# Optimization experiments

Hardware: AMD Instinct MI355X
Metric: run time of the kernel (lower is better)

Reference implementation:

```python
import jax, jax.numpy as jnp
import numpy as np

N = 100000       # nodes
E = 1200000      # edges
D_IN = 64
D_OUT = 64
ALPHA = 0.01     # LeakyReLU negative slope
EPS = 1e-5       # BatchNorm eps


def setup_inputs() -> dict:
    key = jax.random.key(0)
    k0, k1, k2, k3 = jax.random.split(key, 4)
    x = jax.random.normal(k0, (N, D_IN), dtype=jnp.float32)
    edge_idx = jax.random.randint(k1, (2, E), 0, N)
    edge_attr = jax.random.uniform(k2, (E,), dtype=jnp.float32)
    W = jax.random.normal(k3, (D_IN, D_OUT), dtype=jnp.float32) * (1.0 / np.sqrt(D_IN))
    b = jnp.zeros((D_OUT,), dtype=jnp.float32)
    gamma = jnp.ones((D_OUT,), dtype=jnp.float32)
    beta = jnp.zeros((D_OUT,), dtype=jnp.float32)
    return {"x": x, "edge_idx": edge_idx, "edge_attr": edge_attr,
            "W": W, "b": b, "gamma": gamma, "beta": beta}


def reference(x, edge_idx, edge_attr, W, b, gamma, beta):
    n = x.shape[0]
    row, col = edge_idx[0], edge_idx[1]
    # --- GCNConv: add self-loops, symmetric normalization ---
    loops = jnp.arange(n)
    row_f = jnp.concatenate([row, loops])                       # [E+N]
    col_f = jnp.concatenate([col, loops])                       # [E+N]
    w_f = jnp.concatenate([edge_attr, jnp.ones((n,), x.dtype)])  # [E+N]
    deg = jax.ops.segment_sum(w_f, col_f, num_segments=n)       # [N]
    deg_safe = jnp.where(deg > 0, deg, 1.0)
    dis = jnp.where(deg > 0, jax.lax.rsqrt(deg_safe), 0.0)      # deg^-1/2
    norm = dis[row_f] * w_f * dis[col_f]                        # [E+N]
    h = x @ W                                                   # [N, D_OUT]
    msg = norm[:, None] * h[row_f]                              # gather + scale
    agg = jax.ops.segment_sum(msg, col_f, num_segments=n) + b   # scatter-add
    # --- BatchNorm (training-mode batch stats, biased var) ---
    mean = jnp.mean(agg, axis=0)
    var = jnp.mean((agg - mean) ** 2, axis=0)
    hn = (agg - mean) * jax.lax.rsqrt(var + EPS) * gamma + beta
    # --- LeakyReLU ---
    return jnp.where(hn >= 0, hn, ALPHA * hn)
```

## Files before the change

### kernel.cpp

```cpp
#include <hip/hip_runtime.h>

#define D 64
#define ALPHA 0.01f
#define EPS 1e-5f
#define NREP 8
#define CAP 48
#define GSZ 128
#define GMAX 1024
#define NB 256

typedef __attribute__((ext_vector_type(8))) short short8;
typedef __attribute__((ext_vector_type(4))) float f32x4;

__device__ inline unsigned short f2bf(float f) {
    unsigned u = __float_as_uint(f);
    u += 0x7fffu + ((u >> 16) & 1u);
    return (unsigned short)(u >> 16);
}
__device__ inline float bf2f(unsigned short h) { return __uint_as_float((unsigned)h << 16); }

__global__ __launch_bounds__(256) void k_prepA(const float4* __restrict__ x4,
                                               ushort4* __restrict__ xb4,
                                               float* __restrict__ stats,
                                               const int* __restrict__ col,
                                               int* __restrict__ cnt_gb,
                                               long long n16, int G, int E) {
    __shared__ int h[GMAX];
    if (blockIdx.x < NB) {
        int b = blockIdx.x;
        for (int i = threadIdx.x; i < G; i += 256) h[i] = 0;
        __syncthreads();
        int chunk = (E + NB - 1) / NB;
        int e0 = b * chunk;
        int e1 = e0 + chunk; if (e1 > E) e1 = E;
        for (int e = e0 + threadIdx.x; e < e1; e += 256)
            atomicAdd(&h[col[e] >> 7], 1);
        __syncthreads();
        for (int i = threadIdx.x; i < G; i += 256)
            cnt_gb[i * NB + b] = h[i];
    } else {
        long long i = (long long)(blockIdx.x - NB) * 256 + threadIdx.x;
        if (i < n16) {
            float4 v = x4[i];
            ushort4 r;
            r.x = f2bf(v.x); r.y = f2bf(v.y); r.z = f2bf(v.z); r.w = f2bf(v.w);
            xb4[i] = r;
        }
        if (i < NREP * 128) stats[i] = 0.0f;
    }
}

__global__ __launch_bounds__(256) void k_scanA(const int* __restrict__ cnt_gb,
                                               int* __restrict__ bsum, int M) {
    __shared__ int ls[256];
    int base = blockIdx.x * 1024 + threadIdx.x * 4;
    int s = 0;
    if (base + 3 < M) {
        int4 v = *(const int4*)&cnt_gb[base];
        s = v.x + v.y + v.z + v.w;
    } else {
#pragma unroll
        for (int k = 0; k < 4; ++k) { int idx = base + k; if (idx < M) s += cnt_gb[idx]; }
    }
    ls[threadIdx.x] = s;
    __syncthreads();
    for (int off = 128; off > 0; off >>= 1) {
        if (threadIdx.x < off) ls[threadIdx.x] += ls[threadIdx.x + off];
        __syncthreads();
    }
    if (threadIdx.x == 0) bsum[blockIdx.x] = ls[0];
}

__global__ __launch_bounds__(256) void k_scanC(const int* __restrict__ cnt_gb,
                                               const int* __restrict__ bsum,
                                               int* __restrict__ pos,
                                               int* __restrict__ gseg, int M, int G, int E) {
    __shared__ int ls[256];
    int t = threadIdx.x;
    ls[t] = (t < blockIdx.x) ? bsum[t] : 0;
    __syncthreads();
    for (int off = 128; off > 0; off >>= 1) {
        if (t < off) ls[t] += ls[t + off];
        __syncthreads();
    }
    int base_total = ls[0];
    __syncthreads();
    int base = blockIdx.x * 1024 + t * 4;
    int v[4];
    int s = 0;
#pragma unroll
    for (int k = 0; k < 4; ++k) { int idx = base + k; v[k] = (idx < M) ? cnt_gb[idx] : 0; s += v[k]; }
    ls[t] = s;
    __syncthreads();
    int own = s;
    for (int off = 1; off < 256; off <<= 1) {
        int tv = (t >= off) ? ls[t - off] : 0;
        __syncthreads();
        ls[t] += tv;
        __syncthreads();
    }
    int excl = ls[t] - own + base_total;
#pragma unroll
    for (int k = 0; k < 4; ++k) {
        int idx = base + k;
        if (idx < M) {
            pos[idx] = excl;
            if ((idx & (NB - 1)) == 0) gseg[idx >> 8] = excl;
        }
        excl += v[k];
    }
    if (blockIdx.x == 0 && t == 0) gseg[G] = E;
}

__global__ __launch_bounds__(256) void k_binB(const int* __restrict__ eidx,
                                              const float* __restrict__ w,
                                              const int* __restrict__ pos,
                                              uint2* __restrict__ seg, int G, int E) {
    __shared__ int cursor[GMAX];
    int b = blockIdx.x;
    for (int g = threadIdx.x; g < G; g += 256) cursor[g] = pos[g * NB + b];
    __syncthreads();
    int chunk = (E + NB - 1) / NB;
    int e0 = b * chunk;
    int e1 = e0 + chunk; if (e1 > E) e1 = E;
    for (int e = e0 + threadIdx.x; e < e1; e += 256) {
        int row = eidx[e];
        int c = eidx[E + e];
        unsigned wq = (unsigned)(w[e] * 32767.0f + 0.5f);
        int slot = atomicAdd(&cursor[c >> 7], 1);
        seg[slot] = make_uint2((wq << 17) | (unsigned)row, (unsigned)(c & (GSZ - 1)));
    }
}

__global__ __launch_bounds__(256) void k_binC(const uint2* __restrict__ seg,
                                              const int* __restrict__ gseg,
                                              unsigned* __restrict__ bucket,
                                              int* __restrict__ cnt,
                                              float* __restrict__ dis,
                                              float* __restrict__ dis_s, int n) {
    __shared__ int cl[GSZ];
    __shared__ float ws[GSZ];
    int g = blockIdx.x;
    if (threadIdx.x < GSZ) { cl[threadIdx.x] = 0; ws[threadIdx.x] = 0.0f; }
    __syncthreads();
    int s0 = gseg[g], s1 = gseg[g + 1];
    for (int i = s0 + threadIdx.x; i < s1; i += 256) {
        uint2 ev = seg[i];
        int cig = (int)ev.y;
        int rank = atomicAdd(&cl[cig], 1);
        atomicAdd(&ws[cig], (float)(ev.x >> 17) * (1.0f / 32767.0f));
        int node = g * GSZ + cig;
        if (rank < CAP) bucket[(size_t)node * CAP + rank] = ev.x;
    }
    __syncthreads();
    if (threadIdx.x < GSZ) {
        int node = g * GSZ + threadIdx.x;
        if (node < n) {
            cnt[node] = cl[threadIdx.x];
            float d = rsqrtf(1.0f + ws[threadIdx.x]);
            dis[node] = d;
            dis_s[node] = d * (1.0f / 32767.0f);
        }
    }
}

__global__ __launch_bounds__(256) void k_gather(const unsigned short* __restrict__ xb,
                                                const unsigned* __restrict__ bucket,
                                                const int* __restrict__ cnt,
                                                const float* __restrict__ dis,
                                                const float* __restrict__ dis_s,
                                                unsigned short* __restrict__ aggb, int n) {
    int node = blockIdx.x * 4 + (threadIdx.x >> 6);
    if (node >= n) return;
    int lane = threadIdx.x & 63;
    int g = lane >> 3;
    int l = lane & 7;
    int c = cnt[node];
    if (c > CAP) c = CAP;
    float di = dis[node];
    float acc[8] = {0, 0, 0, 0, 0, 0, 0, 0};
    if (g == 0) {
        short8 xv = *(const short8*)(xb + ((size_t)node << 6) + l * 8);
#pragma unroll
        for (int k = 0; k < 8; ++k) acc[k] = bf2f((unsigned short)xv[k]) * di;
    }
    const unsigned* bkt = bucket + (size_t)node * CAP;
    int j0 = g, j1 = g + 8;
    unsigned v0 = (j0 < c) ? bkt[j0] : 0u;
    unsigned v1 = (j1 < c) ? bkt[j1] : 0u;
    while (j0 < c) {
        int p0 = j0 + 16, p1 = j1 + 16;
        unsigned w0 = (p0 < c) ? bkt[p0] : 0u;
        unsigned w1 = (p1 < c) ? bkt[p1] : 0u;
        int s0 = (int)(v0 & 0x1FFFFu);
        int s1 = (int)(v1 & 0x1FFFFu);
        float nr0 = (float)(v0 >> 17) * dis_s[s0];
        float nr1 = (float)(v1 >> 17) * dis_s[s1];
        short8 x0 = *(const short8*)(xb + ((size_t)s0 << 6) + l * 8);
        short8 x1 = *(const short8*)(xb + ((size_t)s1 << 6) + l * 8);
#pragma unroll
        for (int k = 0; k < 8; ++k) acc[k] += nr0 * bf2f((unsigned short)x0[k]);
#pragma unroll
        for (int k = 0; k < 8; ++k) acc[k] += nr1 * bf2f((unsigned short)x1[k]);
        v0 = w0; v1 = w1; j0 = p0; j1 = p1;
    }
#pragma unroll
    for (int off = 8; off <= 32; off <<= 1)
#pragma unroll
        for (int k = 0; k < 8; ++k) acc[k] += __shfl_xor(acc[k], off, 64);
    if (g == 0) {
        short8 r;
#pragma unroll
        for (int k = 0; k < 8; ++k) r[k] = (short)f2bf(acc[k] * di);
        *(short8*)(aggb + ((size_t)node << 6) + l * 8) = r;
    }
}

__global__ __launch_bounds__(256) void k_gemmstats(const unsigned short* __restrict__ aggb,
                                                   const float* __restrict__ Wm,
                                                   float* __restrict__ out,
                                                   float* __restrict__ stats, int n) {
    __shared__ unsigned short Wt[64 * 64];
    __shared__ float ssum[4][64], qsum[4][64];
    int tid = threadIdx.x;
    for (int i = tid; i < 4096; i += 256) {
        int k = i >> 6, nn = i & 63;
        Wt[nn * 64 + k] = f2bf(Wm[i]);
    }
    __syncthreads();
    int wv = tid >> 6;
    int lane = tid & 63;
    int l15 = lane & 15;
    int quad = lane >> 4;

    short8 bfrag[2][4];
#pragma unroll
    for (int h = 0; h < 2; ++h)
#pragma unroll
        for (int g = 0; g < 4; ++g)
            bfrag[h][g] = *(const short8*)&Wt[(g * 16 + l15) * 64 + h * 32 + quad * 8];

    float s[4] = {0, 0, 0, 0}, q[4] = {0, 0, 0, 0};
    int nwt = (n + 15) >> 4;
    for (int wt = blockIdx.x * 4 + wv; wt < nwt; wt += gridDim.x * 4) {
        int row0 = wt * 16;
        int arow = row0 + l15;
        if (arow >= n) arow = n - 1;
        const unsigned short* ap = aggb + (size_t)arow * 64 + quad * 8;
        short8 a0 = *(const short8*)ap;
        short8 a1 = *(const short8*)(ap + 32);
        f32x4 acc[4] = {{0, 0, 0, 0}, {0, 0, 0, 0}, {0, 0, 0, 0}, {0, 0, 0, 0}};
#pragma unroll
        for (int g = 0; g < 4; ++g) {
            acc[g] = __builtin_amdgcn_mfma_f32_16x16x32_bf16(a0, bfrag[0][g], acc[g], 0, 0, 0);
            acc[g] = __builtin_amdgcn_mfma_f32_16x16x32_bf16(a1, bfrag[1][g], acc[g], 0, 0, 0);
        }
#pragma unroll
        for (int r = 0; r < 4; ++r) {
            int row = row0 + quad * 4 + r;
            if (row < n) {
                size_t base = (size_t)row * 64;
#pragma unroll
                for (int g = 0; g < 4; ++g) {
                    float v = acc[g][r];
                    out[base + g * 16 + l15] = v;
                    s[g] += v;
                    q[g] += v * v;
                }
            }
        }
    }
#pragma unroll
    for (int off = 16; off <= 32; off <<= 1) {
#pragma unroll
        for (int g = 0; g < 4; ++g) {
            s[g] += __shfl_xor(s[g], off, 64);
            q[g] += __shfl_xor(q[g], off, 64);
        }
    }
    if (quad == 0) {
#pragma unroll
        for (int g = 0; g < 4; ++g) { ssum[wv][g * 16 + l15] = s[g]; qsum[wv][g * 16 + l15] = q[g]; }
    }
    __syncthreads();
    float* st = stats + (blockIdx.x & (NREP - 1)) * 128;
    if (tid < 64)
        atomicAdd(&st[tid], ssum[0][tid] + ssum[1][tid] + ssum[2][tid] + ssum[3][tid]);
    else if (tid < 128) {
        int t = tid - 64;
        atomicAdd(&st[64 + t], qsum[0][t] + qsum[1][t] + qsum[2][t] + qsum[3][t]);
    }
}

__global__ __launch_bounds__(256) void k_norm(float4* __restrict__ out4,
                                              const float* __restrict__ stats,
                                              const float* __restrict__ gamma,
                                              const float* __restrict__ beta, int n) {
    __shared__ float scale[64], shift[64];
    if (threadIdx.x < 64) {
        float sm = 0.0f, qm = 0.0f;
#pragma unroll
        for (int r = 0; r < NREP; ++r) {
            sm += stats[r * 128 + threadIdx.x];
            qm += stats[r * 128 + 64 + threadIdx.x];
        }
        float inv_n = 1.0f / (float)n;
        float mean = sm * inv_n;
        float var = qm * inv_n - mean * mean;
        float sc = rsqrtf(var + EPS) * gamma[threadIdx.x];
        scale[threadIdx.x] = sc;
        shift[threadIdx.x] = beta[threadIdx.x] - mean * sc;
    }
    __syncthreads();
    long long idx = (long long)blockIdx.x * blockDim.x + threadIdx.x;
    if (idx < (long long)n * 16) {
        int l = (int)(idx & 15);
        float4 v = out4[idx];
        float4 r;
        float a, b2;
        a = scale[l * 4 + 0]; b2 = shift[l * 4 + 0]; r.x = v.x * a + b2; r.x = r.x >= 0.0f ? r.x : ALPHA * r.x;
        a = scale[l * 4 + 1]; b2 = shift[l * 4 + 1]; r.y = v.y * a + b2; r.y = r.y >= 0.0f ? r.y : ALPHA * r.y;
        a = scale[l * 4 + 2]; b2 = shift[l * 4 + 2]; r.z = v.z * a + b2; r.z = r.z >= 0.0f ? r.z : ALPHA * r.z;
        a = scale[l * 4 + 3]; b2 = shift[l * 4 + 3]; r.w = v.w * a + b2; r.w = r.w >= 0.0f ? r.w : ALPHA * r.w;
        out4[idx] = r;
    }
}

extern "C" void kernel_launch(void* const* d_in, const int* in_sizes, int n_in,
                              void* d_out, int out_size, void* d_ws, size_t ws_size,
                              hipStream_t stream) {
    const float* x     = (const float*)d_in[0];
    const int*   eidx  = (const int*)d_in[1];
    const float* eattr = (const float*)d_in[2];
    const float* Wm    = (const float*)d_in[3];
    const float* gamma = (const float*)d_in[5];
    const float* beta  = (const float*)d_in[6];
    float* out = (float*)d_out;

    int n = in_sizes[0] / D;
    int E = in_sizes[2];
    int G = (n + GSZ - 1) / GSZ;
    int M = G * NB;
    int nbs = (M + 1023) / 1024;

    char* p = (char*)d_ws;
    uint2* seg = (uint2*)p;                     p += (size_t)E * 8;
    unsigned* bucket = (unsigned*)p;            p += (size_t)n * CAP * 4;
    unsigned short* xb   = (unsigned short*)p;  p += (size_t)n * D * 2;
    unsigned short* aggb = (unsigned short*)p;  p += (size_t)n * D * 2;
    int* cnt = (int*)p;                         p += (size_t)n * 4;
    float* dis = (float*)p;                     p += (size_t)n * 4;
    float* dis_s = (float*)p;                   p += (size_t)n * 4;
    float* stats = (float*)p;                   p += NREP * 128 * 4;
    int* cnt_gb = (int*)p;                      p += (size_t)M * 4;
    int* pos = (int*)p;                         p += (size_t)M * 4;
    int* gseg = (int*)p;                        p += ((size_t)G + 1) * 4;
    int* bsum = (int*)p;                        p += 256 * 4;

    long long n16 = (long long)n * 16;
    unsigned prep_blocks = (unsigned)((n16 + 255) / 256);

    k_prepA<<<NB + prep_blocks, 256, 0, stream>>>(
        (const float4*)x, (ushort4*)xb, stats, eidx + E, cnt_gb, n16, G, E);
    k_scanA<<<nbs, 256, 0, stream>>>(cnt_gb, bsum, M);
    k_scanC<<<nbs, 256, 0, stream>>>(cnt_gb, bsum, pos, gseg, M, G, E);
    k_binB<<<NB, 256, 0, stream>>>(eidx, eattr, pos, seg, G, E);
    k_binC<<<G, 256, 0, stream>>>(seg, gseg, bucket, cnt, dis, dis_s, n);
    k_gather<<<(n + 3) / 4, 256, 0, stream>>>(xb, bucket, cnt, dis, dis_s, aggb, n);
    k_gemmstats<<<1024, 256, 0, stream>>>(aggb, Wm, out, stats, n);
    k_norm<<<(unsigned)((n16 + 255) / 256), 256, 0, stream>>>(
        (float4*)out, stats, gamma, beta, n);
}
```

Before: 189.7 us.

## Fuse per-node bucketing and gather into group-wise LDS scatter-add aggregation

Drops the per-node capped bucket build (k_binC) and the per-node gather kernel. Each block now handles one 128-node destination group: it seeds a float LDS tile with the self-loop term, then walks that group's edge segment and scatter-adds scaled source rows into the tile with LDS atomics. Weighted degree is accumulated with global integer atomics in k_binB, so the normalization is computed on the fly. This removes a kernel launch, the bucket write/read round trip and the CAP truncation, in exchange for heavy LDS float atomic contention, a scalar per-lane bf16 load per edge, and an extra wdeg lookup per edge.

New measurement: 690.6 us. +264.0%, slower.

```diff
diff --git a/kernel.cpp b/kernel.cpp
--- a/kernel.cpp
+++ b/kernel.cpp
@@ -4,10 +4,10 @@
 #define ALPHA 0.01f
 #define EPS 1e-5f
 #define NREP 8
-#define CAP 48
 #define GSZ 128
 #define GMAX 1024
 #define NB 256
+#define AGG_T 512
 
 typedef __attribute__((ext_vector_type(8))) short short8;
 typedef __attribute__((ext_vector_type(4))) float f32x4;
@@ -24,7 +24,8 @@
                                                float* __restrict__ stats,
                                                const int* __restrict__ col,
                                                int* __restrict__ cnt_gb,
-                                               long long n16, int G, int E) {
+                                               int* __restrict__ wdeg,
+                                               long long n16, int n, int G, int E) {
     __shared__ int h[GMAX];
     if (blockIdx.x < NB) {
         int b = blockIdx.x;
@@ -47,6 +48,7 @@
             xb4[i] = r;
         }
         if (i < NREP * 128) stats[i] = 0.0f;
+        if (i < n) wdeg[i] = 0;
     }
 }
 
@@ -115,6 +117,7 @@
 __global__ __launch_bounds__(256) void k_binB(const int* __restrict__ eidx,
                                               const float* __restrict__ w,
                                               const int* __restrict__ pos,
+                                              int* __restrict__ wdeg,
                                               uint2* __restrict__ seg, int G, int E) {
     __shared__ int cursor[GMAX];
     int b = blockIdx.x;
@@ -127,92 +130,69 @@
         int row = eidx[e];
         int c = eidx[E + e];
         unsigned wq = (unsigned)(w[e] * 32767.0f + 0.5f);
+        atomicAdd(&wdeg[c], (int)wq);
         int slot = atomicAdd(&cursor[c >> 7], 1);
         seg[slot] = make_uint2((wq << 17) | (unsigned)row, (unsigned)(c & (GSZ - 1)));
     }
 }
 
-__global__ __launch_bounds__(256) void k_binC(const uint2* __restrict__ seg,
-                                              const int* __restrict__ gseg,
-                                              unsigned* __restrict__ bucket,
-                                              int* __restrict__ cnt,
-                                              float* __restrict__ dis,
-                                              float* __restrict__ dis_s, int n) {
-    __shared__ int cl[GSZ];
-    __shared__ float ws[GSZ];
-    int g = blockIdx.x;
-    if (threadIdx.x < GSZ) { cl[threadIdx.x] = 0; ws[threadIdx.x] = 0.0f; }
+__global__ __launch_bounds__(AGG_T) void k_agg(const unsigned short* __restrict__ xb,
+                                               const uint2* __restrict__ seg,
+                                               const int* __restrict__ gseg,
+                                               const int* __restrict__ wdeg,
+                                               unsigned short* __restrict__ aggb, int n) {
+    __shared__ float t[GSZ][D];
+    int g = blockIdx.x, tid = threadIdx.x;
+    int base = g * GSZ;
+    for (int i = tid; i < GSZ * 16; i += AGG_T) {
+        int cig = i >> 4, fq = i & 15;
+        int node = base + cig;
+        int nc = node < n ? node : 0;
+        float d = node < n ? rsqrtf(1.0f + (float)wdeg[nc] * (1.0f / 32767.0f)) : 0.0f;
+        ushort4 xv = *(const ushort4*)(xb + ((size_t)nc << 6) + (fq << 2));
+        float4 v;
+        v.x = bf2f(xv.x) * d; v.y = bf2f(xv.y) * d;
+        v.z = bf2f(xv.z) * d; v.w = bf2f(xv.w) * d;
+        *(float4*)&t[cig][fq << 2] = v;
+    }
     __syncthreads();
     int s0 = gseg[g], s1 = gseg[g + 1];
-    for (int i = s0 + threadIdx.x; i < s1; i += 256) {
-        uint2 ev = seg[i];
-        int cig = (int)ev.y;
-        int rank = atomicAdd(&cl[cig], 1);
-        atomicAdd(&ws[cig], (float)(ev.x >> 17) * (1.0f / 32767.0f));
-        int node = g * GSZ + cig;
-        if (rank < CAP) bucket[(size_t)node * CAP + rank] = ev.x;
-    }
-    __syncthreads();
-    if (threadIdx.x < GSZ) {
-        int node = g * GSZ + threadIdx.x;
+    int wv = tid >> 6, lane = tid & 63;
+    for (int eb = s0 + wv * 4; eb < s1; eb += (AGG_T / 64) * 4) {
+        uint2 ev[4];
+#pragma unroll
+        for (int k = 0; k < 4; ++k) {
+            int e = eb + k;
+            ev[k] = (e < s1) ? seg[e] : make_uint2(0u, 0u);
+        }
+        float xv[4], wd[4], wqf[4];
+        int cig[4];
+#pragma unroll
+        for (int k = 0; k < 4; ++k) {
+            int src = (int)(ev[k].x & 0x1FFFFu);
+            wqf[k] = (float)(ev[k].x >> 17);
+            cig[k] = (int)ev[k].y;
+            wd[k] = (float)wdeg[src];
+            xv[k] = bf2f(xb[((size_t)src << 6) + lane]);
+        }
+#pragma unroll
+        for (int k = 0; k < 4; ++k) {
+            float nr = wqf[k] * (1.0f / 32767.0f) * rsqrtf(1.0f + wd[k] * (1.0f / 32767.0f));
+            atomicAdd(&t[cig[k]][lane], nr * xv[k]);
+        }
+    }
+    __syncthreads();
+    for (int i = tid; i < GSZ * 16; i += AGG_T) {
+        int cig = i >> 4, fq = i & 15;
+        int node = base + cig;
         if (node < n) {
-            cnt[node] = cl[threadIdx.x];
-            float d = rsqrtf(1.0f + ws[threadIdx.x]);
-            dis[node] = d;
-            dis_s[node] = d * (1.0f / 32767.0f);
-        }
-    }
-}
-
-__global__ __launch_bounds__(256) void k_gather(const unsigned short* __restrict__ xb,
-                                                const unsigned* __restrict__ bucket,
-                                                const int* __restrict__ cnt,
-                                                const float* __restrict__ dis,
-                                                const float* __restrict__ dis_s,
-                                                unsigned short* __restrict__ aggb, int n) {
-    int node = blockIdx.x * 4 + (threadIdx.x >> 6);
-    if (node >= n) return;
-    int lane = threadIdx.x & 63;
-    int g = lane >> 3;
-    int l = lane & 7;
-    int c = cnt[node];
-    if (c > CAP) c = CAP;
-    float di = dis[node];
-    float acc[8] = {0, 0, 0, 0, 0, 0, 0, 0};
-    if (g == 0) {
-        short8 xv = *(const short8*)(xb + ((size_t)node << 6) + l * 8);
-#pragma unroll
-        for (int k = 0; k < 8; ++k) acc[k] = bf2f((unsigned short)xv[k]) * di;
-    }
-    const unsigned* bkt = bucket + (size_t)node * CAP;
-    int j0 = g, j1 = g + 8;
-    unsigned v0 = (j0 < c) ? bkt[j0] : 0u;
-    unsigned v1 = (j1 < c) ? bkt[j1] : 0u;
-    while (j0 < c) {
-        int p0 = j0 + 16, p1 = j1 + 16;
-        unsigned w0 = (p0 < c) ? bkt[p0] : 0u;
-        unsigned w1 = (p1 < c) ? bkt[p1] : 0u;
-        int s0 = (int)(v0 & 0x1FFFFu);
-        int s1 = (int)(v1 & 0x1FFFFu);
-        float nr0 = (float)(v0 >> 17) * dis_s[s0];
-        float nr1 = (float)(v1 >> 17) * dis_s[s1];
-        short8 x0 = *(const short8*)(xb + ((size_t)s0 << 6) + l * 8);
-        short8 x1 = *(const short8*)(xb + ((size_t)s1 << 6) + l * 8);
-#pragma unroll
-        for (int k = 0; k < 8; ++k) acc[k] += nr0 * bf2f((unsigned short)x0[k]);
-#pragma unroll
-        for (int k = 0; k < 8; ++k) acc[k] += nr1 * bf2f((unsigned short)x1[k]);
-        v0 = w0; v1 = w1; j0 = p0; j1 = p1;
-    }
-#pragma unroll
-    for (int off = 8; off <= 32; off <<= 1)
-#pragma unroll
-        for (int k = 0; k < 8; ++k) acc[k] += __shfl_xor(acc[k], off, 64);
-    if (g == 0) {
-        short8 r;
-#pragma unroll
-        for (int k = 0; k < 8; ++k) r[k] = (short)f2bf(acc[k] * di);
-        *(short8*)(aggb + ((size_t)node << 6) + l * 8) = r;
+            float d = rsqrtf(1.0f + (float)wdeg[node] * (1.0f / 32767.0f));
+            float4 v = *(const float4*)&t[cig][fq << 2];
+            ushort4 r;
+            r.x = f2bf(v.x * d); r.y = f2bf(v.y * d);
+            r.z = f2bf(v.z * d); r.w = f2bf(v.w * d);
+            *(ushort4*)(aggb + ((size_t)node << 6) + (fq << 2)) = r;
+        }
     }
 }
 
@@ -345,12 +325,9 @@
 
     char* p = (char*)d_ws;
     uint2* seg = (uint2*)p;                     p += (size_t)E * 8;
-    unsigned* bucket = (unsigned*)p;            p += (size_t)n * CAP * 4;
     unsigned short* xb   = (unsigned short*)p;  p += (size_t)n * D * 2;
     unsigned short* aggb = (unsigned short*)p;  p += (size_t)n * D * 2;
-    int* cnt = (int*)p;                         p += (size_t)n * 4;
-    float* dis = (float*)p;                     p += (size_t)n * 4;
-    float* dis_s = (float*)p;                   p += (size_t)n * 4;
+    int* wdeg = (int*)p;                        p += (size_t)n * 4;
     float* stats = (float*)p;                   p += NREP * 128 * 4;
     int* cnt_gb = (int*)p;                      p += (size_t)M * 4;
     int* pos = (int*)p;                         p += (size_t)M * 4;
@@ -361,12 +338,11 @@
     unsigned prep_blocks = (unsigned)((n16 + 255) / 256);
 
     k_prepA<<<NB + prep_blocks, 256, 0, stream>>>(
-        (const float4*)x, (ushort4*)xb, stats, eidx + E, cnt_gb, n16, G, E);
+        (const float4*)x, (ushort4*)xb, stats, eidx + E, cnt_gb, wdeg, n16, n, G, E);
     k_scanA<<<nbs, 256, 0, stream>>>(cnt_gb, bsum, M);
     k_scanC<<<nbs, 256, 0, stream>>>(cnt_gb, bsum, pos, gseg, M, G, E);
-    k_binB<<<NB, 256, 0, stream>>>(eidx, eattr, pos, seg, G, E);
-    k_binC<<<G, 256, 0, stream>>>(seg, gseg, bucket, cnt, dis, dis_s, n);
-    k_gather<<<(n + 3) / 4, 256, 0, stream>>>(xb, bucket, cnt, dis, dis_s, aggb, n);
+    k_binB<<<NB, 256, 0, stream>>>(eidx, eattr, pos, wdeg, seg, G, E);
+    k_agg<<<G, AGG_T, 0, stream>>>(xb, seg, gseg, wdeg, aggb, n);
     k_gemmstats<<<1024, 256, 0, stream>>>(aggb, Wm, out, stats, n);
     k_norm<<<(unsigned)((n16 + 255) / 256), 256, 0, stream>>>(
         (float4*)out, stats, gamma, beta, n);
```

## Restructure gather to one lane per feature with 16-edge batched loads

Applied to the files above, without the earlier changes.

The gather kernel now assigns one lane per output feature instead of splitting the wavefront into 8 edge groups of 8 lanes. Each wave reads bucket entries as uint4 vectors 16 at a time and issues 16 independent scalar bf16 loads per lane, which removes the cross-group shuffle reduction. The aim is more memory-level parallelism and no reduction overhead. In exchange, every wave loads the same bucket words, the per-lane loads are narrower (2 bytes instead of 16), and padding entries past the count still trigger loads of node 0.

Result: slower. 204.6 us (+7.8%).

```diff
diff --git a/kernel.cpp b/kernel.cpp
--- a/kernel.cpp
+++ b/kernel.cpp
@@ -173,47 +173,34 @@
     int node = blockIdx.x * 4 + (threadIdx.x >> 6);
     if (node >= n) return;
     int lane = threadIdx.x & 63;
-    int g = lane >> 3;
-    int l = lane & 7;
     int c = cnt[node];
     if (c > CAP) c = CAP;
     float di = dis[node];
-    float acc[8] = {0, 0, 0, 0, 0, 0, 0, 0};
-    if (g == 0) {
-        short8 xv = *(const short8*)(xb + ((size_t)node << 6) + l * 8);
-#pragma unroll
-        for (int k = 0; k < 8; ++k) acc[k] = bf2f((unsigned short)xv[k]) * di;
-    }
-    const unsigned* bkt = bucket + (size_t)node * CAP;
-    int j0 = g, j1 = g + 8;
-    unsigned v0 = (j0 < c) ? bkt[j0] : 0u;
-    unsigned v1 = (j1 < c) ? bkt[j1] : 0u;
-    while (j0 < c) {
-        int p0 = j0 + 16, p1 = j1 + 16;
-        unsigned w0 = (p0 < c) ? bkt[p0] : 0u;
-        unsigned w1 = (p1 < c) ? bkt[p1] : 0u;
-        int s0 = (int)(v0 & 0x1FFFFu);
-        int s1 = (int)(v1 & 0x1FFFFu);
-        float nr0 = (float)(v0 >> 17) * dis_s[s0];
-        float nr1 = (float)(v1 >> 17) * dis_s[s1];
-        short8 x0 = *(const short8*)(xb + ((size_t)s0 << 6) + l * 8);
-        short8 x1 = *(const short8*)(xb + ((size_t)s1 << 6) + l * 8);
-#pragma unroll
-        for (int k = 0; k < 8; ++k) acc[k] += nr0 * bf2f((unsigned short)x0[k]);
-#pragma unroll
-        for (int k = 0; k < 8; ++k) acc[k] += nr1 * bf2f((unsigned short)x1[k]);
-        v0 = w0; v1 = w1; j0 = p0; j1 = p1;
-    }
-#pragma unroll
-    for (int off = 8; off <= 32; off <<= 1)
-#pragma unroll
-        for (int k = 0; k < 8; ++k) acc[k] += __shfl_xor(acc[k], off, 64);
-    if (g == 0) {
-        short8 r;
-#pragma unroll
-        for (int k = 0; k < 8; ++k) r[k] = (short)f2bf(acc[k] * di);
-        *(short8*)(aggb + ((size_t)node << 6) + l * 8) = r;
-    }
+    float acc = bf2f(xb[((size_t)node << 6) + lane]) * di;
+    const uint4* bkt4 = (const uint4*)(bucket + (size_t)node * CAP);
+    for (int j0 = 0; j0 < c; j0 += 16) {
+        uint4 q0 = bkt4[(j0 >> 2) + 0];
+        uint4 q1 = bkt4[(j0 >> 2) + 1];
+        uint4 q2 = bkt4[(j0 >> 2) + 2];
+        uint4 q3 = bkt4[(j0 >> 2) + 3];
+        unsigned e[16];
+        e[0]  = q0.x; e[1]  = q0.y; e[2]  = q0.z; e[3]  = q0.w;
+        e[4]  = q1.x; e[5]  = q1.y; e[6]  = q1.z; e[7]  = q1.w;
+        e[8]  = q2.x; e[9]  = q2.y; e[10] = q2.z; e[11] = q2.w;
+        e[12] = q3.x; e[13] = q3.y; e[14] = q3.z; e[15] = q3.w;
+        int rem = c - j0;
+        float xv[16], nr[16];
+#pragma unroll
+        for (int k = 0; k < 16; ++k) {
+            unsigned ek = (k < rem) ? e[k] : 0u;
+            int s = (int)(ek & 0x1FFFFu);
+            xv[k] = bf2f(xb[((size_t)s << 6) + lane]);
+            nr[k] = (float)(ek >> 17) * dis_s[s];
+        }
+#pragma unroll
+        for (int k = 0; k < 16; ++k) acc += nr[k] * xv[k];
+    }
+    aggb[((size_t)node << 6) + lane] = f2bf(acc * di);
 }
 
 __global__ __launch_bounds__(256) void k_gemmstats(const unsigned short* __restrict__ aggb,
```

## Recompute GEMM in BN pass instead of storing and reloading fp32 output

Applied to the files above, without the earlier changes.

The stats kernel no longer writes the fp32 pre-norm output; it only accumulates column sums and sums of squares. A new kernel reloads the bf16 aggregated features, redoes the small 64x64 MFMA GEMM, and applies BatchNorm and LeakyReLU before a single fp32 store. This drops one fp32 write and one fp32 read-modify-write of the output (about 25.6MB each) in exchange for reading the bf16 input twice and running the GEMM twice.

Measured after the change: 188.5 us. About the same (-0.6%).

```diff
diff --git a/kernel.cpp b/kernel.cpp
--- a/kernel.cpp
+++ b/kernel.cpp
@@ -218,7 +218,6 @@
 
 __global__ __launch_bounds__(256) void k_gemmstats(const unsigned short* __restrict__ aggb,
                                                    const float* __restrict__ Wm,
-                                                   float* __restrict__ out,
                                                    float* __restrict__ stats, int n) {
     __shared__ unsigned short Wt[64 * 64];
     __shared__ float ssum[4][64], qsum[4][64];
@@ -259,11 +258,9 @@
         for (int r = 0; r < 4; ++r) {
             int row = row0 + quad * 4 + r;
             if (row < n) {
-                size_t base = (size_t)row * 64;
 #pragma unroll
                 for (int g = 0; g < 4; ++g) {
                     float v = acc[g][r];
-                    out[base + g * 16 + l15] = v;
                     s[g] += v;
                     q[g] += v * v;
                 }
@@ -292,37 +289,76 @@
     }
 }
 
-__global__ __launch_bounds__(256) void k_norm(float4* __restrict__ out4,
-                                              const float* __restrict__ stats,
-                                              const float* __restrict__ gamma,
-                                              const float* __restrict__ beta, int n) {
+__global__ __launch_bounds__(256) void k_gemmbn(const unsigned short* __restrict__ aggb,
+                                                const float* __restrict__ Wm,
+                                                float* __restrict__ out,
+                                                const float* __restrict__ stats,
+                                                const float* __restrict__ gamma,
+                                                const float* __restrict__ beta, int n) {
+    __shared__ unsigned short Wt[64 * 64];
     __shared__ float scale[64], shift[64];
-    if (threadIdx.x < 64) {
+    int tid = threadIdx.x;
+    for (int i = tid; i < 4096; i += 256) {
+        int k = i >> 6, nn = i & 63;
+        Wt[nn * 64 + k] = f2bf(Wm[i]);
+    }
+    if (tid < 64) {
         float sm = 0.0f, qm = 0.0f;
 #pragma unroll
         for (int r = 0; r < NREP; ++r) {
-            sm += stats[r * 128 + threadIdx.x];
-            qm += stats[r * 128 + 64 + threadIdx.x];
+            sm += stats[r * 128 + tid];
+            qm += stats[r * 128 + 64 + tid];
         }
         float inv_n = 1.0f / (float)n;
         float mean = sm * inv_n;
         float var = qm * inv_n - mean * mean;
-        float sc = rsqrtf(var + EPS) * gamma[threadIdx.x];
-        scale[threadIdx.x] = sc;
-        shift[threadIdx.x] = beta[threadIdx.x] - mean * sc;
-    }
-    __syncthreads();
-    long long idx = (long long)blockIdx.x * blockDim.x + threadIdx.x;
-    if (idx < (long long)n * 16) {
-        int l = (int)(idx & 15);
-        float4 v = out4[idx];
-        float4 r;
-        float a, b2;
-        a = scale[l * 4 + 0]; b2 = shift[l * 4 + 0]; r.x = v.x * a + b2; r.x = r.x >= 0.0f ? r.x : ALPHA * r.x;
-        a = scale[l * 4 + 1]; b2 = shift[l * 4 + 1]; r.y = v.y * a + b2; r.y = r.y >= 0.0f ? r.y : ALPHA * r.y;
-        a = scale[l * 4 + 2]; b2 = shift[l * 4 + 2]; r.z = v.z * a + b2; r.z = r.z >= 0.0f ? r.z : ALPHA * r.z;
-        a = scale[l * 4 + 3]; b2 = shift[l * 4 + 3]; r.w = v.w * a + b2; r.w = r.w >= 0.0f ? r.w : ALPHA * r.w;
-        out4[idx] = r;
+        float sc = rsqrtf(var + EPS) * gamma[tid];
+        scale[tid] = sc;
+        shift[tid] = beta[tid] - mean * sc;
+    }
+    __syncthreads();
+    int wv = tid >> 6;
+    int lane = tid & 63;
+    int l15 = lane & 15;
+    int quad = lane >> 4;
+
+    short8 bfrag[2][4];
+    float bsc[4], bsh[4];
+#pragma unroll
+    for (int h = 0; h < 2; ++h)
+#pragma unroll
+        for (int g = 0; g < 4; ++g)
+            bfrag[h][g] = *(const short8*)&Wt[(g * 16 + l15) * 64 + h * 32 + quad * 8];
+#pragma unroll
+    for (int g = 0; g < 4; ++g) { bsc[g] = scale[g * 16 + l15]; bsh[g] = shift[g * 16 + l15]; }
+
+    int nwt = (n + 15) >> 4;
+    for (int wt = blockIdx.x * 4 + wv; wt < nwt; wt += gridDim.x * 4) {
+        int row0 = wt * 16;
+        int arow = row0 + l15;
+        if (arow >= n) arow = n - 1;
+        const unsigned short* ap = aggb + (size_t)arow * 64 + quad * 8;
+        short8 a0 = *(const short8*)ap;
+        short8 a1 = *(const short8*)(ap + 32);
+        f32x4 acc[4] = {{0, 0, 0, 0}, {0, 0, 0, 0}, {0, 0, 0, 0}, {0, 0, 0, 0}};
+#pragma unroll
+        for (int g = 0; g < 4; ++g) {
+            acc[g] = __builtin_amdgcn_mfma_f32_16x16x32_bf16(a0, bfrag[0][g], acc[g], 0, 0, 0);
+            acc[g] = __builtin_amdgcn_mfma_f32_16x16x32_bf16(a1, bfrag[1][g], acc[g], 0, 0, 0);
+        }
+#pragma unroll
+        for (int r = 0; r < 4; ++r) {
+            int row = row0 + quad * 4 + r;
+            if (row < n) {
+                size_t base = (size_t)row * 64;
+#pragma unroll
+                for (int g = 0; g < 4; ++g) {
+                    float v = acc[g][r] * bsc[g] + bsh[g];
+                    v = v >= 0.0f ? v : ALPHA * v;
+                    out[base + g * 16 + l15] = v;
+                }
+            }
+        }
     }
 }
 
@@ -367,7 +403,6 @@
     k_binB<<<NB, 256, 0, stream>>>(eidx, eattr, pos, seg, G, E);
     k_binC<<<G, 256, 0, stream>>>(seg, gseg, bucket, cnt, dis, dis_s, n);
     k_gather<<<(n + 3) / 4, 256, 0, stream>>>(xb, bucket, cnt, dis, dis_s, aggb, n);
-    k_gemmstats<<<1024, 256, 0, stream>>>(aggb, Wm, out, stats, n);
-    k_norm<<<(unsigned)((n16 + 255) / 256), 256, 0, stream>>>(
-        (float4*)out, stats, gamma, beta, n);
-}
+    k_gemmstats<<<1024, 256, 0, stream>>>(aggb, Wm, stats, n);
+    k_gemmbn<<<1024, 256, 0, stream>>>(aggb, Wm, out, stats, gamma, beta, n);
+}
```
